# Kernel tuning notes

Measured on AMD Instinct MI355X. Metric: run time of the kernel, lower is better.

Reference implementation:

```python
import jax, jax.numpy as jnp
import numpy as np

NUM_HEADS = 8
NUM_POINTS = 4


def setup_inputs() -> dict:
    key = jax.random.key(0)
    bs, h, w = 2, 128, 128
    cin = cout = 256
    nq = h * w
    ks = jax.random.split(key, 6)
    query = jax.random.normal(ks[0], (bs, nq, cin), jnp.float32)
    value = jax.random.normal(ks[1], (bs, nq, cin), jnp.float32)
    # sampling_offsets: small random weight, bias = directional grid init (as in init_weights)
    W_off = jax.random.normal(ks[2], (cin, NUM_HEADS * NUM_POINTS * 2), jnp.float32) * 0.01
    thetas = np.arange(NUM_HEADS, dtype=np.float32) * (2.0 * np.pi / NUM_HEADS)
    grid = np.stack([np.cos(thetas), np.sin(thetas)], -1)
    grid = grid / np.abs(grid).max(-1, keepdims=True)
    grid = np.tile(grid[:, None, :], (1, NUM_POINTS, 1)) * (np.arange(NUM_POINTS, dtype=np.float32)[None, :, None] + 1.0)
    b_off = jnp.asarray(grid.reshape(-1), jnp.float32)
    W_attn = jax.random.normal(ks[3], (cin, NUM_HEADS * NUM_POINTS), jnp.float32) * 0.01
    b_attn = jnp.zeros((NUM_HEADS * NUM_POINTS,), jnp.float32)
    s = 1.0 / np.sqrt(cin)  # xavier-ish uniform
    W_val = jax.random.uniform(ks[4], (cin, cout), jnp.float32, -s, s)
    b_val = jnp.zeros((cout,), jnp.float32)
    W_out = jax.random.uniform(ks[5], (cout, cout), jnp.float32, -s, s)
    b_out = jnp.zeros((cout,), jnp.float32)
    return {"query": query, "value": value, "W_off": W_off, "b_off": b_off,
            "W_attn": W_attn, "b_attn": b_attn, "W_val": W_val, "b_val": b_val,
            "W_out": W_out, "b_out": b_out, "h": h, "w": w}


def _bilinear_sample(v_flat, ix, iy, h, w):
    # v_flat: (bs, heads, h*w, d); ix/iy: (bs, heads, nq, P) pixel coords.
    # grid_sample bilinear, align_corners=False, padding_mode='zeros'.
    x0 = jnp.floor(ix)
    y0 = jnp.floor(iy)
    wx1 = ix - x0
    wy1 = iy - y0
    bs, hd, nq, P = ix.shape
    acc = 0.0
    corners = ((x0, y0, (1.0 - wx1) * (1.0 - wy1)),
               (x0 + 1.0, y0, wx1 * (1.0 - wy1)),
               (x0, y0 + 1.0, (1.0 - wx1) * wy1),
               (x0 + 1.0, y0 + 1.0, wx1 * wy1))
    for xc, yc, wgt in corners:
        xi = xc.astype(jnp.int32)
        yi = yc.astype(jnp.int32)
        valid = (xi >= 0) & (xi < w) & (yi >= 0) & (yi < h)
        idx = jnp.clip(yi, 0, h - 1) * w + jnp.clip(xi, 0, w - 1)
        g = jnp.take_along_axis(v_flat, idx.reshape(bs, hd, nq * P)[..., None], axis=2)
        acc = acc + g.reshape(bs, hd, nq, P, -1) * (wgt * valid)[..., None]
    return acc  # (bs, heads, nq, P, d)


def deform_attn(query, value, W_off, b_off, W_attn, b_attn, W_val, b_val, h, w):
    bs, nq, _ = query.shape
    d = W_val.shape[1] // NUM_HEADS
    v = (value @ W_val + b_val).reshape(bs, nq, NUM_HEADS, d)
    off = (query @ W_off + b_off).reshape(bs, nq, NUM_HEADS, NUM_POINTS, 2)
    aw = jax.nn.softmax((query @ W_attn + b_attn).reshape(bs, nq, NUM_HEADS, NUM_POINTS), axis=-1)
    # reference points in [0,1], scale_ratio=1.0, (x, y) order
    ys = (jnp.arange(h, dtype=jnp.float32) + 0.5) / h
    xs = (jnp.arange(w, dtype=jnp.float32) + 0.5) / w
    ry, rx = jnp.meshgrid(ys, xs, indexing='ij')
    ref = jnp.stack([rx.reshape(-1), ry.reshape(-1)], -1)  # (nq, 2)
    loc = ref[None, :, None, None, :] + off / jnp.array([w, h], jnp.float32)
    grid = 2.0 * loc - 1.0  # normalized grid_sample coords
    grid = grid.transpose(0, 2, 1, 3, 4)  # (bs, heads, nq, P, 2)
    ix = (grid[..., 0] + 1.0) * (w / 2.0) - 0.5
    iy = (grid[..., 1] + 1.0) * (h / 2.0) - 0.5
    v_flat = v.transpose(0, 2, 1, 3)  # (bs, heads, h*w, d)
    sampled = _bilinear_sample(v_flat, ix, iy, h, w)  # (bs, heads, nq, P, d)
    out = (sampled * aw.transpose(0, 2, 1, 3)[..., None]).sum(3)  # (bs, heads, nq, d)
    return out.transpose(0, 2, 1, 3).reshape(bs, nq, NUM_HEADS * d)


def reference(query, value, W_off, b_off, W_attn, b_attn, W_val, b_val, W_out, b_out, h, w):
    attn = deform_attn(query, value, W_off, b_off, W_attn, b_attn, W_val, b_val, h, w)
    # dropout acts as identity in eval mode; identity residual = query
    return attn @ W_out + b_out + query
```

## Files before the change

kernel.cpp:

```cpp
#include <hip/hip_runtime.h>

#define H_IMG 128
#define W_IMG 128
#define NQ (H_IMG * W_IMG)
#define CIN 256
#define NH 8
#define NP 4
#define DH 32
#define LDSP 264

typedef __bf16 bf16x4 __attribute__((ext_vector_type(4)));
typedef __bf16 bf16x8 __attribute__((ext_vector_type(8)));
typedef float f32x4 __attribute__((ext_vector_type(4)));

__global__ __launch_bounds__(256) void prep_weights(
    const float* __restrict__ Wval, const float* __restrict__ Wout,
    const float* __restrict__ Woff, const float* __restrict__ Wattn,
    const float* __restrict__ boff, const float* __restrict__ battn,
    __bf16* __restrict__ btv, __bf16* __restrict__ bto,
    __bf16* __restrict__ btoa, float* __restrict__ bias96) {
  int id = blockIdx.x * 256 + threadIdx.x;
  if (id < 256 * 256) {
    int n = id >> 8, k = id & 255;
    btv[n * 256 + k] = (__bf16)Wval[k * 256 + n];
    bto[n * 256 + k] = (__bf16)Wout[k * 256 + n];
  }
  if (id < 96 * 256) {
    int n = id >> 8, k = id & 255;
    float w = (n < 64) ? Woff[k * 64 + n] : Wattn[k * 32 + (n - 64)];
    btoa[n * 256 + k] = (__bf16)w;
  }
  if (id < 96) {
    bias96[id] = (id < 64) ? boff[id] : battn[id - 64];
  }
}

__global__ __launch_bounds__(256) void gemm_v(
    const float* __restrict__ A, const __bf16* __restrict__ BT,
    const float* __restrict__ bias, __bf16* __restrict__ v, int M) {
  const int t = threadIdx.x;
  const int lane = t & 63;
  const int wave = t >> 6;
  const int r = lane & 15;
  const int q = lane >> 4;
  const int gm0 = blockIdx.x * 64;
  const int wn = wave * 64;

  __shared__ __bf16 As[64 * LDSP];

#pragma unroll
  for (int i = 0; i < 16; ++i) {
    int g = i * 256 + t;
    int row = g >> 6, c4 = g & 63;
    float4 f = *(const float4*)(A + (size_t)(gm0 + row) * 256 + c4 * 4);
    bf16x4 hh;
    hh[0] = (__bf16)f.x; hh[1] = (__bf16)f.y;
    hh[2] = (__bf16)f.z; hh[3] = (__bf16)f.w;
    *(bf16x4*)(&As[row * LDSP + c4 * 4]) = hh;
  }
  __syncthreads();

  f32x4 acc[4][4];
#pragma unroll
  for (int mt = 0; mt < 4; ++mt)
#pragma unroll
    for (int nt = 0; nt < 4; ++nt) acc[mt][nt] = (f32x4){0.f, 0.f, 0.f, 0.f};

#pragma unroll
  for (int kt = 0; kt < 8; ++kt) {
    const int ko = kt * 32 + q * 8;
    bf16x8 a[4], b[4];
#pragma unroll
    for (int mt = 0; mt < 4; ++mt)
      a[mt] = *(const bf16x8*)(&As[(mt * 16 + r) * LDSP + ko]);
#pragma unroll
    for (int nt = 0; nt < 4; ++nt)
      b[nt] = *(const bf16x8*)(BT + (size_t)(wn + nt * 16 + r) * 256 + ko);
#pragma unroll
    for (int mt = 0; mt < 4; ++mt)
#pragma unroll
      for (int nt = 0; nt < 4; ++nt)
        acc[mt][nt] =
            __builtin_amdgcn_mfma_f32_16x16x32_bf16(a[mt], b[nt], acc[mt][nt], 0, 0, 0);
  }

#pragma unroll
  for (int mt = 0; mt < 4; ++mt)
#pragma unroll
    for (int nt = 0; nt < 4; ++nt)
#pragma unroll
      for (int rr = 0; rr < 4; ++rr) {
        int row = gm0 + mt * 16 + q * 4 + rr;
        int col = wn + nt * 16 + r;
        v[((size_t)(col >> 5) * M + row) * 32 + (col & 31)] =
            (__bf16)(acc[mt][nt][rr] + bias[col]);
      }
}

__global__ __launch_bounds__(256, 2) void oa_sample_out(
    const float* __restrict__ query, const __bf16* __restrict__ btoa,
    const float* __restrict__ bias96, const __bf16* __restrict__ v,
    const __bf16* __restrict__ bto, const float* __restrict__ b_out,
    float* __restrict__ out, int M) {
  const int t = threadIdx.x;
  const int lane = t & 63;
  const int wave = t >> 6;
  const int r = lane & 15;
  const int q = lane >> 4;
  const int gm0 = blockIdx.x * 64;

  __shared__ __bf16 As[64 * LDSP];
  __shared__ float oas[64 * 100];

#pragma unroll
  for (int i = 0; i < 16; ++i) {
    int g = i * 256 + t;
    int row = g >> 6, c4 = g & 63;
    float4 f = *(const float4*)(query + (size_t)(gm0 + row) * 256 + c4 * 4);
    bf16x4 hh;
    hh[0] = (__bf16)f.x; hh[1] = (__bf16)f.y;
    hh[2] = (__bf16)f.z; hh[3] = (__bf16)f.w;
    *(bf16x4*)(&As[row * LDSP + c4 * 4]) = hh;
  }
  __syncthreads();

  {
    const int wm = (wave & 1) * 32;
    const int n0 = (wave >> 1) * 48;
    f32x4 acc[2][3];
#pragma unroll
    for (int mt = 0; mt < 2; ++mt)
#pragma unroll
      for (int nt = 0; nt < 3; ++nt) acc[mt][nt] = (f32x4){0.f, 0.f, 0.f, 0.f};
#pragma unroll
    for (int kt = 0; kt < 8; ++kt) {
      const int ko = kt * 32 + q * 8;
      bf16x8 a0 = *(const bf16x8*)(&As[(wm + r) * LDSP + ko]);
      bf16x8 a1 = *(const bf16x8*)(&As[(wm + 16 + r) * LDSP + ko]);
      bf16x8 b[3];
#pragma unroll
      for (int nt = 0; nt < 3; ++nt)
        b[nt] = *(const bf16x8*)(btoa + (size_t)(n0 + nt * 16 + r) * 256 + ko);
#pragma unroll
      for (int nt = 0; nt < 3; ++nt) {
        acc[0][nt] = __builtin_amdgcn_mfma_f32_16x16x32_bf16(a0, b[nt], acc[0][nt], 0, 0, 0);
        acc[1][nt] = __builtin_amdgcn_mfma_f32_16x16x32_bf16(a1, b[nt], acc[1][nt], 0, 0, 0);
      }
    }
#pragma unroll
    for (int mt = 0; mt < 2; ++mt)
#pragma unroll
      for (int nt = 0; nt < 3; ++nt)
#pragma unroll
        for (int rr = 0; rr < 4; ++rr) {
          int rl = wm + mt * 16 + q * 4 + rr;
          int col = n0 + nt * 16 + r;
          oas[rl * 100 + col] = acc[mt][nt][rr] + bias96[col];
        }
  }
  __syncthreads();

  {
    const int qrow = t >> 2;
    const int c8 = (t & 3) * 8;
    const int row = gm0 + qrow;
    const int b = row >> 14;
    const int qi = row & (NQ - 1);
    const int x = qi & (W_IMG - 1);
    const int y = qi >> 7;
    const float* oar = &oas[qrow * 100];
#pragma unroll
    for (int h = 0; h < NH; ++h) {
      float l0 = oar[64 + h * 4 + 0];
      float l1 = oar[64 + h * 4 + 1];
      float l2 = oar[64 + h * 4 + 2];
      float l3 = oar[64 + h * 4 + 3];
      float mx = fmaxf(fmaxf(l0, l1), fmaxf(l2, l3));
      float e0 = __expf(l0 - mx), e1 = __expf(l1 - mx);
      float e2 = __expf(l2 - mx), e3 = __expf(l3 - mx);
      float inv = 1.f / (e0 + e1 + e2 + e3);
      float awp[4] = {e0 * inv, e1 * inv, e2 * inv, e3 * inv};

      int offs[16];
      float wvs[16];
#pragma unroll
      for (int p = 0; p < NP; ++p) {
        float ox = oar[h * 8 + p * 2 + 0];
        float oy = oar[h * 8 + p * 2 + 1];
        float ix = (float)x + ox;
        float iy = (float)y + oy;
        float x0f = floorf(ix), y0f = floorf(iy);
        float wx1 = ix - x0f, wy1 = iy - y0f;
        int x0 = (int)x0f, y0 = (int)y0f;
        float wgt[4] = {(1.f - wx1) * (1.f - wy1), wx1 * (1.f - wy1),
                        (1.f - wx1) * wy1, wx1 * wy1};
        int xs[4] = {x0, x0 + 1, x0, x0 + 1};
        int ysv[4] = {y0, y0, y0 + 1, y0 + 1};
#pragma unroll
        for (int c = 0; c < 4; ++c) {
          int xi = xs[c], yi = ysv[c];
          bool valid = (xi >= 0) & (xi < W_IMG) & (yi >= 0) & (yi < H_IMG);
          int xc = xi < 0 ? 0 : (xi > W_IMG - 1 ? W_IMG - 1 : xi);
          int yc = yi < 0 ? 0 : (yi > H_IMG - 1 ? H_IMG - 1 : yi);
          offs[p * 4 + c] = (yc * W_IMG + xc) * (DH * 2);
          wvs[p * 4 + c] = awp[p] * wgt[c] * (valid ? 1.f : 0.f);
        }
      }

      const char* vb =
          (const char*)v + ((size_t)h * M + (size_t)b * NQ) * (DH * 2) + c8 * 2;
      bf16x8 g[16];
#pragma unroll
      for (int i = 0; i < 16; ++i) g[i] = *(const bf16x8*)(vb + offs[i]);

      float fa[8] = {0.f, 0.f, 0.f, 0.f, 0.f, 0.f, 0.f, 0.f};
#pragma unroll
      for (int i = 0; i < 16; ++i) {
        float wv = wvs[i];
#pragma unroll
        for (int j = 0; j < 8; ++j) fa[j] += wv * (float)g[i][j];
      }

      bf16x8 o;
#pragma unroll
      for (int j = 0; j < 8; ++j) o[j] = (__bf16)fa[j];
      *(bf16x8*)(&As[qrow * LDSP + h * DH + c8]) = o;
    }
  }
  __syncthreads();

  {
    const int wn = wave * 64;
    f32x4 acc[4][4];
#pragma unroll
    for (int mt = 0; mt < 4; ++mt)
#pragma unroll
      for (int nt = 0; nt < 4; ++nt) acc[mt][nt] = (f32x4){0.f, 0.f, 0.f, 0.f};
#pragma unroll
    for (int kt = 0; kt < 8; ++kt) {
      const int ko = kt * 32 + q * 8;
      bf16x8 a[4], b[4];
#pragma unroll
      for (int mt = 0; mt < 4; ++mt)
        a[mt] = *(const bf16x8*)(&As[(mt * 16 + r) * LDSP + ko]);
#pragma unroll
      for (int nt = 0; nt < 4; ++nt)
        b[nt] = *(const bf16x8*)(bto + (size_t)(wn + nt * 16 + r) * 256 + ko);
#pragma unroll
      for (int mt = 0; mt < 4; ++mt)
#pragma unroll
        for (int nt = 0; nt < 4; ++nt)
          acc[mt][nt] =
              __builtin_amdgcn_mfma_f32_16x16x32_bf16(a[mt], b[nt], acc[mt][nt], 0, 0, 0);
    }
#pragma unroll
    for (int mt = 0; mt < 4; ++mt)
#pragma unroll
      for (int nt = 0; nt < 4; ++nt)
#pragma unroll
        for (int rr = 0; rr < 4; ++rr) {
          int row = gm0 + mt * 16 + q * 4 + rr;
          int col = wn + nt * 16 + r;
          out[(size_t)row * 256 + col] =
              acc[mt][nt][rr] + b_out[col] + query[(size_t)row * 256 + col];
        }
  }
}

extern "C" void kernel_launch(void* const* d_in, const int* in_sizes, int n_in,
                              void* d_out, int out_size, void* d_ws, size_t ws_size,
                              hipStream_t stream) {
  const float* query  = (const float*)d_in[0];
  const float* value  = (const float*)d_in[1];
  const float* W_off  = (const float*)d_in[2];
  const float* b_off  = (const float*)d_in[3];
  const float* W_attn = (const float*)d_in[4];
  const float* b_attn = (const float*)d_in[5];
  const float* W_val  = (const float*)d_in[6];
  const float* b_val  = (const float*)d_in[7];
  const float* W_out  = (const float*)d_in[8];
  const float* b_out  = (const float*)d_in[9];
  float* out = (float*)d_out;

  char* ws = (char*)d_ws;
  __bf16* btv    = (__bf16*)(ws + 0);
  __bf16* bto    = (__bf16*)(ws + 131072);
  __bf16* btoa   = (__bf16*)(ws + 262144);
  float*  bias96 = (float*)(ws + 311296);
  __bf16* v      = (__bf16*)(ws + 524288);

  const int M = in_sizes[0] / CIN;

  prep_weights<<<256, 256, 0, stream>>>(W_val, W_out, W_off, W_attn,
                                        b_off, b_attn, btv, bto, btoa, bias96);
  gemm_v<<<M / 64, 256, 0, stream>>>(value, btv, b_val, v, M);
  oa_sample_out<<<M / 64, 256, 0, stream>>>(query, btoa, bias96, v, bto, b_out, out, M);
}
```

Before: 165.1 us.

## Halve query tile to 32 rows and split heads across thread groups

```diff
diff --git a/kernel.cpp b/kernel.cpp
--- a/kernel.cpp
+++ b/kernel.cpp
@@ -8,6 +8,7 @@
 #define NP 4
 #define DH 32
 #define LDSP 264
+#define QB 32
 
 typedef __bf16 bf16x4 __attribute__((ext_vector_type(4)));
 typedef __bf16 bf16x8 __attribute__((ext_vector_type(8)));
@@ -107,13 +108,13 @@
   const int wave = t >> 6;
   const int r = lane & 15;
   const int q = lane >> 4;
-  const int gm0 = blockIdx.x * 64;
-
-  __shared__ __bf16 As[64 * LDSP];
-  __shared__ float oas[64 * 100];
-
-#pragma unroll
-  for (int i = 0; i < 16; ++i) {
+  const int gm0 = blockIdx.x * QB;
+
+  __shared__ __bf16 As[QB * LDSP];
+  __shared__ float oas[QB * 100];
+
+#pragma unroll
+  for (int i = 0; i < 8; ++i) {
     int g = i * 256 + t;
     int row = g >> 6, c4 = g & 63;
     float4 f = *(const float4*)(query + (size_t)(gm0 + row) * 256 + c4 * 4);
@@ -125,43 +126,38 @@
   __syncthreads();
 
   {
-    const int wm = (wave & 1) * 32;
+    const int wm = (wave & 1) * 16;
     const int n0 = (wave >> 1) * 48;
-    f32x4 acc[2][3];
-#pragma unroll
-    for (int mt = 0; mt < 2; ++mt)
-#pragma unroll
-      for (int nt = 0; nt < 3; ++nt) acc[mt][nt] = (f32x4){0.f, 0.f, 0.f, 0.f};
+    f32x4 acc[3];
+#pragma unroll
+    for (int nt = 0; nt < 3; ++nt) acc[nt] = (f32x4){0.f, 0.f, 0.f, 0.f};
 #pragma unroll
     for (int kt = 0; kt < 8; ++kt) {
       const int ko = kt * 32 + q * 8;
-      bf16x8 a0 = *(const bf16x8*)(&As[(wm + r) * LDSP + ko]);
-      bf16x8 a1 = *(const bf16x8*)(&As[(wm + 16 + r) * LDSP + ko]);
+      bf16x8 a = *(const bf16x8*)(&As[(wm + r) * LDSP + ko]);
       bf16x8 b[3];
 #pragma unroll
       for (int nt = 0; nt < 3; ++nt)
         b[nt] = *(const bf16x8*)(btoa + (size_t)(n0 + nt * 16 + r) * 256 + ko);
 #pragma unroll
-      for (int nt = 0; nt < 3; ++nt) {
-        acc[0][nt] = __builtin_amdgcn_mfma_f32_16x16x32_bf16(a0, b[nt], acc[0][nt], 0, 0, 0);
-        acc[1][nt] = __builtin_amdgcn_mfma_f32_16x16x32_bf16(a1, b[nt], acc[1][nt], 0, 0, 0);
-      }
+      for (int nt = 0; nt < 3; ++nt)
+        acc[nt] = __builtin_amdgcn_mfma_f32_16x16x32_bf16(a, b[nt], acc[nt], 0, 0, 0);
     }
 #pragma unroll
-    for (int mt = 0; mt < 2; ++mt)
-#pragma unroll
-      for (int nt = 0; nt < 3; ++nt)
-#pragma unroll
-        for (int rr = 0; rr < 4; ++rr) {
-          int rl = wm + mt * 16 + q * 4 + rr;
-          int col = n0 + nt * 16 + r;
-          oas[rl * 100 + col] = acc[mt][nt][rr] + bias96[col];
-        }
+    for (int nt = 0; nt < 3; ++nt)
+#pragma unroll
+      for (int rr = 0; rr < 4; ++rr) {
+        int rl = wm + q * 4 + rr;
+        int col = n0 + nt * 16 + r;
+        oas[rl * 100 + col] = acc[nt][rr] + bias96[col];
+      }
   }
   __syncthreads();
 
   {
-    const int qrow = t >> 2;
+    const int slot = t >> 2;
+    const int qrow = slot & (QB - 1);
+    const int hgrp = slot >> 5;
     const int c8 = (t & 3) * 8;
     const int row = gm0 + qrow;
     const int b = row >> 14;
@@ -170,7 +166,8 @@
     const int y = qi >> 7;
     const float* oar = &oas[qrow * 100];
 #pragma unroll
-    for (int h = 0; h < NH; ++h) {
+    for (int hh_ = 0; hh_ < 4; ++hh_) {
+      const int h = hgrp * 4 + hh_;
       float l0 = oar[64 + h * 4 + 0];
       float l1 = oar[64 + h * 4 + 1];
       float l2 = oar[64 + h * 4 + 2];
@@ -231,30 +228,30 @@
 
   {
     const int wn = wave * 64;
-    f32x4 acc[4][4];
-#pragma unroll
-    for (int mt = 0; mt < 4; ++mt)
+    f32x4 acc[2][4];
+#pragma unroll
+    for (int mt = 0; mt < 2; ++mt)
 #pragma unroll
       for (int nt = 0; nt < 4; ++nt) acc[mt][nt] = (f32x4){0.f, 0.f, 0.f, 0.f};
 #pragma unroll
     for (int kt = 0; kt < 8; ++kt) {
       const int ko = kt * 32 + q * 8;
-      bf16x8 a[4], b[4];
-#pragma unroll
-      for (int mt = 0; mt < 4; ++mt)
+      bf16x8 a[2], b[4];
+#pragma unroll
+      for (int mt = 0; mt < 2; ++mt)
         a[mt] = *(const bf16x8*)(&As[(mt * 16 + r) * LDSP + ko]);
 #pragma unroll
       for (int nt = 0; nt < 4; ++nt)
         b[nt] = *(const bf16x8*)(bto + (size_t)(wn + nt * 16 + r) * 256 + ko);
 #pragma unroll
-      for (int mt = 0; mt < 4; ++mt)
+      for (int mt = 0; mt < 2; ++mt)
 #pragma unroll
         for (int nt = 0; nt < 4; ++nt)
           acc[mt][nt] =
               __builtin_amdgcn_mfma_f32_16x16x32_bf16(a[mt], b[nt], acc[mt][nt], 0, 0, 0);
     }
 #pragma unroll
-    for (int mt = 0; mt < 4; ++mt)
+    for (int mt = 0; mt < 2; ++mt)
 #pragma unroll
       for (int nt = 0; nt < 4; ++nt)
 #pragma unroll
@@ -294,5 +291,5 @@
   prep_weights<<<256, 256, 0, stream>>>(W_val, W_out, W_off, W_attn,
                                         b_off, b_attn, btv, bto, btoa, bias96);
   gemm_v<<<M / 64, 256, 0, stream>>>(value, btv, b_val, v, M);
-  oa_sample_out<<<M / 64, 256, 0, stream>>>(query, btoa, bias96, v, bto, b_out, out, M);
-}
+  oa_sample_out<<<M / QB, 256, 0, stream>>>(query, btoa, bias96, v, bto, b_out, out, M);
+}
```

Result: slower. 170.5 us (+3.3%).
